# Kernel optimization log

Measured on AMD Instinct MI355X. Metric: run time of the kernel, lower is better.

## Reference

```python
import jax, jax.numpy as jnp
import numpy as np

POSE_IDS = np.array([0, 4, 8, 12, 16])
BN_EPS = 1e-5


def setup_inputs() -> dict:
    key = jax.random.key(0)
    ks = jax.random.split(key, 8)
    N, C, H, W = 64, 2048, 24, 12
    P, Cl = 5, 256
    Cm = C + P * Cl  # 3328
    return {
        "x": jax.random.normal(ks[0], (N, C, H, W), jnp.float32),
        "poses": jax.random.uniform(ks[1], (N, 17, 4), jnp.float32),
        "local_w": jax.random.normal(ks[2], (P, Cl, C), jnp.float32) * 0.02,
        "local_b": jnp.zeros((P, Cl), jnp.float32),
        "local_gamma": jnp.ones((P, Cl), jnp.float32),
        "local_beta": jnp.zeros((P, Cl), jnp.float32),
        "local_mean": jax.random.normal(ks[3], (P, Cl), jnp.float32) * 0.1,
        "local_var": jax.random.uniform(ks[4], (P, Cl), jnp.float32, 0.5, 1.5),
        "merge_w": jax.random.normal(ks[5], (C, Cm), jnp.float32) * 0.02,
        "merge_b": jnp.zeros((C,), jnp.float32),
        "merge_gamma": jnp.ones((C,), jnp.float32),
        "merge_beta": jnp.zeros((C,), jnp.float32),
        "merge_mean": jax.random.normal(ks[6], (C,), jnp.float32) * 0.1,
        "merge_var": jax.random.uniform(ks[7], (C,), jnp.float32, 0.5, 1.5),
    }


def reference(x, poses, local_w, local_b, local_gamma, local_beta, local_mean,
              local_var, merge_w, merge_b, merge_gamma, merge_beta, merge_mean,
              merge_var):
    N, C, H, W = x.shape
    kp = poses[:, jnp.asarray(POSE_IDS), :]  # [N,P,4]
    # box = [left, top, w, h]; clamp to [0, 0.75]; scale whole box by confidence
    half = jnp.full_like(kp[..., 0], 0.5)
    box = jnp.stack([kp[..., 0] - 0.25, kp[..., 1] - 0.25, half, half], axis=-1)
    box = jnp.clip(box, 0.0, 0.75) * kp[..., 2:3]
    # integer ROI bounds on the feature grid (round-half-to-even like torch)
    xs = jnp.maximum(0, jnp.round(W * box[..., 0])).astype(jnp.int32)          # [N,P]
    xe = jnp.minimum(W - 1, jnp.round(W * (box[..., 0] + box[..., 2]))).astype(jnp.int32)
    ys = jnp.maximum(0, jnp.round(H * box[..., 1])).astype(jnp.int32)
    ye = jnp.minimum(H - 1, jnp.round(H * (box[..., 1] + box[..., 3]))).astype(jnp.int32)
    rows = jnp.arange(H)
    cols = jnp.arange(W)
    mh = (rows[None, None, :] >= ys[..., None]) & (rows[None, None, :] < ye[..., None])  # [N,P,H]
    mw = (cols[None, None, :] >= xs[..., None]) & (cols[None, None, :] < xe[..., None])  # [N,P,W]
    mask = (mh[..., :, None] & mw[..., None, :]).astype(x.dtype)  # [N,P,H,W]
    # masked average pool over the ROI (single pass over x)
    sums = jnp.einsum('nchw,nphw->npc', x, mask)
    area = ((ye - ys) * (xe - xs)).astype(x.dtype)
    avg = sums / jnp.where(area > 0, area, 1.0)[..., None]  # [N,P,C], 0 for empty ROIs
    # per-part 1x1 conv + BN(eval) + ReLU -> [N,P,Cl]
    loc = jnp.einsum('npc,pkc->npk', avg, local_w) + local_b[None]
    loc = (loc - local_mean[None]) * (local_gamma[None] / jnp.sqrt(local_var[None] + BN_EPS)) + local_beta[None]
    loc = jax.nn.relu(loc)
    # global max pool -> [N,C]
    gfeat = x.max(axis=(2, 3))
    cat = jnp.concatenate([loc.reshape(N, -1), gfeat], axis=1)  # [N, P*Cl + C]
    # merge 1x1 conv + BN(eval) + ReLU
    y = cat @ merge_w.T + merge_b
    y = (y - merge_mean) * (merge_gamma / jnp.sqrt(merge_var + BN_EPS)) + merge_beta
    y = jax.nn.relu(y)
    # F.normalize(p=2, dim=1)
    norm = jnp.linalg.norm(y, axis=1, keepdims=True)
    return y / jnp.maximum(norm, 1e-12)
```

## Files before the change

kernel.cpp:

```cpp
#include <hip/hip_runtime.h>

#define N_   64
#define C_   2048
#define HW_  288
#define P_   5
#define CM_  3328
#define LOC_ 1280
#define SEGC 8
#define SEGM 13

#define PITCH  28
#define WPITCH 72

typedef __attribute__((ext_vector_type(8))) short bf16x8;
typedef __attribute__((ext_vector_type(4))) float f32x4;

__device__ __forceinline__ unsigned short f2bf(float f) {
  unsigned u = __float_as_uint(f);
  u = (u + 0x7FFFu + ((u >> 16) & 1u)) >> 16;
  return (unsigned short)u;
}
__device__ __forceinline__ unsigned pack2(float lo, float hi) {
  return (unsigned)f2bf(lo) | ((unsigned)f2bf(hi) << 16);
}

__global__ __launch_bounds__(256) void kB(const float* __restrict__ x,
    const float* __restrict__ poses,
    unsigned short* __restrict__ avgB, unsigned short* __restrict__ catB) {
  __shared__ float lds[2][256 * PITCH];
  const int t  = threadIdx.x;
  const int n  = blockIdx.x >> 3;
  const int cb = (blockIdx.x & 7) << 8;
  const int chbase = n * C_ + cb;

  unsigned MH[P_], MW[P_];
  float INV[P_];
  const float* kpn = poses + (size_t)n * 68;
#pragma unroll
  for (int p = 0; p < P_; ++p) {
    const float* kp = kpn + 16 * p;
    float px = kp[0], py = kp[1], z = kp[2];
    float bx = fminf(fmaxf(px - 0.25f, 0.f), 0.75f) * z;
    float by = fminf(fmaxf(py - 0.25f, 0.f), 0.75f) * z;
    float bw = 0.5f * z;
    float bh = 0.5f * z;
    int xs = (int)fmaxf(0.f,  rintf(12.f * bx));
    int xe = (int)fminf(11.f, rintf(12.f * (bx + bw)));
    int ys = (int)fmaxf(0.f,  rintf(24.f * by));
    int ye = (int)fminf(23.f, rintf(24.f * (by + bh)));
    MH[p] = ((1u << ye) - 1u) & ~((1u << ys) - 1u);
    MW[p] = ((1u << xe) - 1u) & ~((1u << xs) - 1u);
    int area = (ye - ys) * (xe - xs);
    INV[p] = area > 0 ? 1.f / (float)area : 1.f;
  }

  const float4* x4 = (const float4*)x;
  size_t gbase[6];
  int    loff[6];
#pragma unroll
  for (int k = 0; k < 6; ++k) {
    unsigned flat = k * 256 + t;
    unsigned cl = flat / 6u;
    unsigned j  = flat - 6u * cl;
    gbase[k] = (size_t)(chbase + cl) * 72 + j;
    loff[k]  = cl * PITCH + 4 * j;
  }

  float4 rg[6];
  auto loadRegs = [&](int ci) {
#pragma unroll
    for (int k = 0; k < 6; ++k) rg[k] = x4[gbase[k] + ci * 6];
  };
  auto writeRegs = [&](int db) {
#pragma unroll
    for (int k = 0; k < 6; ++k) *(float4*)&lds[db][loff[k]] = rg[k];
  };

  float s[P_] = {0.f, 0.f, 0.f, 0.f, 0.f};
  float mx = -3.402823466e+38f;

  loadRegs(0);
  writeRegs(0);
  __syncthreads();
  for (int ci = 0; ci < 12; ++ci) {
    if (ci + 1 < 12) loadRegs(ci + 1);
    const float* row = &lds[ci & 1][t * PITCH];
#pragma unroll
    for (int r = 0; r < 2; ++r) {
      int h = 2 * ci + r;
      float4 a = *(const float4*)(row + r * 12 + 0);
      float4 b = *(const float4*)(row + r * 12 + 4);
      float4 c = *(const float4*)(row + r * 12 + 8);
      float m1 = fmaxf(fmaxf(a.x, a.y), fmaxf(a.z, a.w));
      float m2 = fmaxf(fmaxf(b.x, b.y), fmaxf(b.z, b.w));
      float m3 = fmaxf(fmaxf(c.x, c.y), fmaxf(c.z, c.w));
      mx = fmaxf(mx, fmaxf(m1, fmaxf(m2, m3)));
#pragma unroll
      for (int p = 0; p < P_; ++p) {
        unsigned cm = ((MH[p] >> h) & 1u) ? MW[p] : 0u;
        if (cm) {
          float t0 = ((cm & 0x001u) ? a.x : 0.f) + ((cm & 0x002u) ? a.y : 0.f);
          float t1 = ((cm & 0x004u) ? a.z : 0.f) + ((cm & 0x008u) ? a.w : 0.f);
          float t2 = ((cm & 0x010u) ? b.x : 0.f) + ((cm & 0x020u) ? b.y : 0.f);
          float t3 = ((cm & 0x040u) ? b.z : 0.f) + ((cm & 0x080u) ? b.w : 0.f);
          float t4 = ((cm & 0x100u) ? c.x : 0.f) + ((cm & 0x200u) ? c.y : 0.f);
          float t5 = ((cm & 0x400u) ? c.z : 0.f) + ((cm & 0x800u) ? c.w : 0.f);
          s[p] += ((t0 + t1) + (t2 + t3)) + (t4 + t5);
        }
      }
    }
    if (ci + 1 < 12) {
      writeRegs((ci + 1) & 1);
      __syncthreads();
    }
  }

  int c = cb + t;
  catB[(size_t)n * CM_ + LOC_ + c] = f2bf(mx);
#pragma unroll
  for (int p = 0; p < P_; ++p)
    avgB[((size_t)n * 5 + p) * C_ + c] = f2bf(s[p] * INV[p]);
}

__device__ __forceinline__ void mfma_seg(const uint4* __restrict__ aRow,
                                         const float4* __restrict__ wRow,
                                         unsigned short* As, unsigned short* Ws,
                                         f32x4 acc[4]) {
  const int t  = threadIdx.x;
  const int kq = t & 3;
  const int row = t >> 2;
  const int w  = t >> 6;
  const int l  = t & 63;
  unsigned short* aw = &As[row * WPITCH + kq * 16];
  unsigned short* ww = &Ws[row * WPITCH + kq * 16];
  const int arow16 = (16 * w + (l & 15)) * WPITCH + (l >> 4) * 8;
  const int brow16 = (l & 15) * WPITCH + (l >> 4) * 8;
  for (int g = 0; g < 4; ++g) {
    uint4 a0 = aRow[g * 8 + 0], a1 = aRow[g * 8 + 1];
    float4 w0 = wRow[g * 16 + 0], w1 = wRow[g * 16 + 1],
           w2 = wRow[g * 16 + 2], w3 = wRow[g * 16 + 3];
    uint4 pw0, pw1;
    pw0.x = pack2(w0.x, w0.y); pw0.y = pack2(w0.z, w0.w);
    pw0.z = pack2(w1.x, w1.y); pw0.w = pack2(w1.z, w1.w);
    pw1.x = pack2(w2.x, w2.y); pw1.y = pack2(w2.z, w2.w);
    pw1.z = pack2(w3.x, w3.y); pw1.w = pack2(w3.z, w3.w);
    if (g) __syncthreads();
    *(uint4*)aw = a0; *(uint4*)(aw + 8) = a1;
    *(uint4*)ww = pw0; *(uint4*)(ww + 8) = pw1;
    __syncthreads();
#pragma unroll
    for (int s = 0; s < 2; ++s) {
      bf16x8 af = *(const bf16x8*)&As[arow16 + s * 32];
#pragma unroll
      for (int jm = 0; jm < 4; ++jm) {
        bf16x8 bf = *(const bf16x8*)&Ws[jm * 16 * WPITCH + brow16 + s * 32];
        acc[jm] = __builtin_amdgcn_mfma_f32_16x16x32_bf16(af, bf, acc[jm], 0, 0, 0);
      }
    }
  }
}

__global__ __launch_bounds__(256) void kC(const unsigned short* __restrict__ avgB,
                                          const float* __restrict__ local_w,
                                          float* __restrict__ locP) {
  __shared__ unsigned short As[64 * WPITCH];
  __shared__ unsigned short Ws[64 * WPITCH];
  int b  = blockIdx.x;
  int p  = b >> 5;
  int kt = (b >> 3) & 3;
  int sg = b & 7;
  const int t = threadIdx.x, row = t >> 2, kq = t & 3, w = t >> 6, l = t & 63;
  const uint4*  aRow = (const uint4*)avgB + ((size_t)row * 5 + p) * 256 + sg * 32 + kq * 2;
  const float4* wRow = (const float4*)(local_w + ((size_t)p * 256 + kt * 64 + row) * C_
                                       + sg * 256 + kq * 16);
  f32x4 acc[4] = {{0,0,0,0},{0,0,0,0},{0,0,0,0},{0,0,0,0}};
  mfma_seg(aRow, wRow, As, Ws, acc);
  float* outp = locP + (size_t)sg * (N_ * LOC_);
#pragma unroll
  for (int jm = 0; jm < 4; ++jm)
#pragma unroll
    for (int r = 0; r < 4; ++r)
      outp[(size_t)(16 * w + (l >> 4) * 4 + r) * LOC_ + p * 256 + kt * 64 + jm * 16 + (l & 15)]
        = acc[jm][r];
}

__global__ __launch_bounds__(256) void kC2(const float* __restrict__ locP,
    const float* __restrict__ lb, const float* __restrict__ lg, const float* __restrict__ lbe,
    const float* __restrict__ lm, const float* __restrict__ lv,
    unsigned short* __restrict__ catB) {
  int i = blockIdx.x * 256 + threadIdx.x;
  int n = i / LOC_;
  int q = i - n * LOC_;
  float s = 0.f;
#pragma unroll
  for (int sg = 0; sg < SEGC; ++sg) s += locP[(size_t)sg * (N_ * LOC_) + i];
  float sc = lg[q] / sqrtf(lv[q] + 1e-5f);
  float v = (s + lb[q] - lm[q]) * sc + lbe[q];
  catB[(size_t)n * CM_ + q] = f2bf(fmaxf(v, 0.f));
}

__global__ __launch_bounds__(256) void kD(const unsigned short* __restrict__ catB,
                                          const float* __restrict__ merge_w,
                                          float* __restrict__ mrgP) {
  __shared__ unsigned short As[64 * WPITCH];
  __shared__ unsigned short Ws[64 * WPITCH];
  int b  = blockIdx.x;
  int jt = b / SEGM;
  int sg = b - jt * SEGM;
  const int t = threadIdx.x, row = t >> 2, kq = t & 3, w = t >> 6, l = t & 63;
  const uint4*  aRow = (const uint4*)catB + (size_t)row * 416 + sg * 32 + kq * 2;
  const float4* wRow = (const float4*)(merge_w + (size_t)(jt * 64 + row) * CM_
                                       + sg * 256 + kq * 16);
  f32x4 acc[4] = {{0,0,0,0},{0,0,0,0},{0,0,0,0},{0,0,0,0}};
  mfma_seg(aRow, wRow, As, Ws, acc);
  float* outp = mrgP + (size_t)sg * (N_ * C_);
#pragma unroll
  for (int jm = 0; jm < 4; ++jm)
#pragma unroll
    for (int r = 0; r < 4; ++r)
      outp[(size_t)(16 * w + (l >> 4) * 4 + r) * C_ + jt * 64 + jm * 16 + (l & 15)]
        = acc[jm][r];
}

__global__ __launch_bounds__(256) void kE(const float* __restrict__ mrgP,
    const float* __restrict__ mb, const float* __restrict__ mg, const float* __restrict__ mbe,
    const float* __restrict__ mm, const float* __restrict__ mv,
    float* __restrict__ out) {
  int n = blockIdx.x, t = threadIdx.x;
  float z[8]; float ss = 0.f;
#pragma unroll
  for (int r = 0; r < 8; ++r) {
    int j = t + (r << 8);
    float y = 0.f;
#pragma unroll
    for (int sg = 0; sg < SEGM; ++sg) y += mrgP[(size_t)sg * (N_ * C_) + (size_t)n * C_ + j];
    float sc = mg[j] / sqrtf(mv[j] + 1e-5f);
    float v = (y + mb[j] - mm[j]) * sc + mbe[j];
    v = fmaxf(v, 0.f);
    z[r] = v; ss += v * v;
  }
#pragma unroll
  for (int off = 32; off; off >>= 1) ss += __shfl_xor(ss, off, 64);
  __shared__ float red[4];
  if ((t & 63) == 0) red[t >> 6] = ss;
  __syncthreads();
  float tot = red[0] + red[1] + red[2] + red[3];
  float inv = 1.f / fmaxf(sqrtf(tot), 1e-12f);
#pragma unroll
  for (int r = 0; r < 8; ++r) out[(size_t)n * C_ + t + (r << 8)] = z[r] * inv;
}

extern "C" void kernel_launch(void* const* d_in, const int* in_sizes, int n_in,
                              void* d_out, int out_size, void* d_ws, size_t ws_size,
                              hipStream_t stream) {
  const float* x          = (const float*)d_in[0];
  const float* poses      = (const float*)d_in[1];
  const float* local_w    = (const float*)d_in[2];
  const float* local_b    = (const float*)d_in[3];
  const float* local_g    = (const float*)d_in[4];
  const float* local_be   = (const float*)d_in[5];
  const float* local_m    = (const float*)d_in[6];
  const float* local_v    = (const float*)d_in[7];
  const float* merge_w    = (const float*)d_in[8];
  const float* merge_b    = (const float*)d_in[9];
  const float* merge_g    = (const float*)d_in[10];
  const float* merge_be   = (const float*)d_in[11];
  const float* merge_m    = (const float*)d_in[12];
  const float* merge_v    = (const float*)d_in[13];

  char* ws = (char*)d_ws;
  unsigned short* catB = (unsigned short*)ws;
  unsigned short* avgB = (unsigned short*)(ws + 425984);
  float* locP = (float*)(ws + 1736704);
  float* mrgP = (float*)(ws + 4358144);

  kB<<<512, 256, 0, stream>>>(x, poses, avgB, catB);
  kC<<<20 * SEGC, 256, 0, stream>>>(avgB, local_w, locP);
  kC2<<<(N_ * LOC_) / 256, 256, 0, stream>>>(locP, local_b, local_g, local_be,
                                             local_m, local_v, catB);
  kD<<<32 * SEGM, 256, 0, stream>>>(catB, merge_w, mrgP);
  kE<<<N_, 256, 0, stream>>>(mrgP, merge_b, merge_g, merge_be, merge_m, merge_v,
                             (float*)d_out);
}
```

Measured before the change: 294.7 us.

## Fuse all five stages into one cooperative persistent kernel with grid syncs

Replaces the five separate kernel launches with a single cooperative kernel of 256 blocks that runs each stage in turn, separated by grid-wide barriers. The aim is to remove launch overhead and the gaps between kernels. In exchange, the pooling and merge-GEMM stages now loop over work units with only 256 blocks instead of 512/416. That can lower parallelism and latency hiding, and the grid syncs add their own cost.

```diff
diff --git a/kernel.cpp b/kernel.cpp
--- a/kernel.cpp
+++ b/kernel.cpp
@@ -1,8 +1,10 @@
 #include <hip/hip_runtime.h>
+#include <hip/hip_cooperative_groups.h>
+
+namespace cg = cooperative_groups;
 
 #define N_   64
 #define C_   2048
-#define HW_  288
 #define P_   5
 #define CM_  3328
 #define LOC_ 1280
@@ -22,104 +24,6 @@
 }
 __device__ __forceinline__ unsigned pack2(float lo, float hi) {
   return (unsigned)f2bf(lo) | ((unsigned)f2bf(hi) << 16);
-}
-
-__global__ __launch_bounds__(256) void kB(const float* __restrict__ x,
-    const float* __restrict__ poses,
-    unsigned short* __restrict__ avgB, unsigned short* __restrict__ catB) {
-  __shared__ float lds[2][256 * PITCH];
-  const int t  = threadIdx.x;
-  const int n  = blockIdx.x >> 3;
-  const int cb = (blockIdx.x & 7) << 8;
-  const int chbase = n * C_ + cb;
-
-  unsigned MH[P_], MW[P_];
-  float INV[P_];
-  const float* kpn = poses + (size_t)n * 68;
-#pragma unroll
-  for (int p = 0; p < P_; ++p) {
-    const float* kp = kpn + 16 * p;
-    float px = kp[0], py = kp[1], z = kp[2];
-    float bx = fminf(fmaxf(px - 0.25f, 0.f), 0.75f) * z;
-    float by = fminf(fmaxf(py - 0.25f, 0.f), 0.75f) * z;
-    float bw = 0.5f * z;
-    float bh = 0.5f * z;
-    int xs = (int)fmaxf(0.f,  rintf(12.f * bx));
-    int xe = (int)fminf(11.f, rintf(12.f * (bx + bw)));
-    int ys = (int)fmaxf(0.f,  rintf(24.f * by));
-    int ye = (int)fminf(23.f, rintf(24.f * (by + bh)));
-    MH[p] = ((1u << ye) - 1u) & ~((1u << ys) - 1u);
-    MW[p] = ((1u << xe) - 1u) & ~((1u << xs) - 1u);
-    int area = (ye - ys) * (xe - xs);
-    INV[p] = area > 0 ? 1.f / (float)area : 1.f;
-  }
-
-  const float4* x4 = (const float4*)x;
-  size_t gbase[6];
-  int    loff[6];
-#pragma unroll
-  for (int k = 0; k < 6; ++k) {
-    unsigned flat = k * 256 + t;
-    unsigned cl = flat / 6u;
-    unsigned j  = flat - 6u * cl;
-    gbase[k] = (size_t)(chbase + cl) * 72 + j;
-    loff[k]  = cl * PITCH + 4 * j;
-  }
-
-  float4 rg[6];
-  auto loadRegs = [&](int ci) {
-#pragma unroll
-    for (int k = 0; k < 6; ++k) rg[k] = x4[gbase[k] + ci * 6];
-  };
-  auto writeRegs = [&](int db) {
-#pragma unroll
-    for (int k = 0; k < 6; ++k) *(float4*)&lds[db][loff[k]] = rg[k];
-  };
-
-  float s[P_] = {0.f, 0.f, 0.f, 0.f, 0.f};
-  float mx = -3.402823466e+38f;
-
-  loadRegs(0);
-  writeRegs(0);
-  __syncthreads();
-  for (int ci = 0; ci < 12; ++ci) {
-    if (ci + 1 < 12) loadRegs(ci + 1);
-    const float* row = &lds[ci & 1][t * PITCH];
-#pragma unroll
-    for (int r = 0; r < 2; ++r) {
-      int h = 2 * ci + r;
-      float4 a = *(const float4*)(row + r * 12 + 0);
-      float4 b = *(const float4*)(row + r * 12 + 4);
-      float4 c = *(const float4*)(row + r * 12 + 8);
-      float m1 = fmaxf(fmaxf(a.x, a.y), fmaxf(a.z, a.w));
-      float m2 = fmaxf(fmaxf(b.x, b.y), fmaxf(b.z, b.w));
-      float m3 = fmaxf(fmaxf(c.x, c.y), fmaxf(c.z, c.w));
-      mx = fmaxf(mx, fmaxf(m1, fmaxf(m2, m3)));
-#pragma unroll
-      for (int p = 0; p < P_; ++p) {
-        unsigned cm = ((MH[p] >> h) & 1u) ? MW[p] : 0u;
-        if (cm) {
-          float t0 = ((cm & 0x001u) ? a.x : 0.f) + ((cm & 0x002u) ? a.y : 0.f);
-          float t1 = ((cm & 0x004u) ? a.z : 0.f) + ((cm & 0x008u) ? a.w : 0.f);
-          float t2 = ((cm & 0x010u) ? b.x : 0.f) + ((cm & 0x020u) ? b.y : 0.f);
-          float t3 = ((cm & 0x040u) ? b.z : 0.f) + ((cm & 0x080u) ? b.w : 0.f);
-          float t4 = ((cm & 0x100u) ? c.x : 0.f) + ((cm & 0x200u) ? c.y : 0.f);
-          float t5 = ((cm & 0x400u) ? c.z : 0.f) + ((cm & 0x800u) ? c.w : 0.f);
-          s[p] += ((t0 + t1) + (t2 + t3)) + (t4 + t5);
-        }
-      }
-    }
-    if (ci + 1 < 12) {
-      writeRegs((ci + 1) & 1);
-      __syncthreads();
-    }
-  }
-
-  int c = cb + t;
-  catB[(size_t)n * CM_ + LOC_ + c] = f2bf(mx);
-#pragma unroll
-  for (int p = 0; p < P_; ++p)
-    avgB[((size_t)n * 5 + p) * C_ + c] = f2bf(s[p] * INV[p]);
 }
 
 __device__ __forceinline__ void mfma_seg(const uint4* __restrict__ aRow,
@@ -144,7 +48,7 @@
     pw0.z = pack2(w1.x, w1.y); pw0.w = pack2(w1.z, w1.w);
     pw1.x = pack2(w2.x, w2.y); pw1.y = pack2(w2.z, w2.w);
     pw1.z = pack2(w3.x, w3.y); pw1.w = pack2(w3.z, w3.w);
-    if (g) __syncthreads();
+    __syncthreads();
     *(uint4*)aw = a0; *(uint4*)(aw + 8) = a1;
     *(uint4*)ww = pw0; *(uint4*)(ww + 8) = pw1;
     __syncthreads();
@@ -160,94 +64,205 @@
   }
 }
 
-__global__ __launch_bounds__(256) void kC(const unsigned short* __restrict__ avgB,
-                                          const float* __restrict__ local_w,
-                                          float* __restrict__ locP) {
-  __shared__ unsigned short As[64 * WPITCH];
-  __shared__ unsigned short Ws[64 * WPITCH];
-  int b  = blockIdx.x;
-  int p  = b >> 5;
-  int kt = (b >> 3) & 3;
-  int sg = b & 7;
-  const int t = threadIdx.x, row = t >> 2, kq = t & 3, w = t >> 6, l = t & 63;
-  const uint4*  aRow = (const uint4*)avgB + ((size_t)row * 5 + p) * 256 + sg * 32 + kq * 2;
-  const float4* wRow = (const float4*)(local_w + ((size_t)p * 256 + kt * 64 + row) * C_
-                                       + sg * 256 + kq * 16);
-  f32x4 acc[4] = {{0,0,0,0},{0,0,0,0},{0,0,0,0},{0,0,0,0}};
-  mfma_seg(aRow, wRow, As, Ws, acc);
-  float* outp = locP + (size_t)sg * (N_ * LOC_);
-#pragma unroll
-  for (int jm = 0; jm < 4; ++jm)
-#pragma unroll
-    for (int r = 0; r < 4; ++r)
-      outp[(size_t)(16 * w + (l >> 4) * 4 + r) * LOC_ + p * 256 + kt * 64 + jm * 16 + (l & 15)]
-        = acc[jm][r];
-}
-
-__global__ __launch_bounds__(256) void kC2(const float* __restrict__ locP,
-    const float* __restrict__ lb, const float* __restrict__ lg, const float* __restrict__ lbe,
-    const float* __restrict__ lm, const float* __restrict__ lv,
-    unsigned short* __restrict__ catB) {
-  int i = blockIdx.x * 256 + threadIdx.x;
-  int n = i / LOC_;
-  int q = i - n * LOC_;
-  float s = 0.f;
-#pragma unroll
-  for (int sg = 0; sg < SEGC; ++sg) s += locP[(size_t)sg * (N_ * LOC_) + i];
-  float sc = lg[q] / sqrtf(lv[q] + 1e-5f);
-  float v = (s + lb[q] - lm[q]) * sc + lbe[q];
-  catB[(size_t)n * CM_ + q] = f2bf(fmaxf(v, 0.f));
-}
-
-__global__ __launch_bounds__(256) void kD(const unsigned short* __restrict__ catB,
-                                          const float* __restrict__ merge_w,
-                                          float* __restrict__ mrgP) {
-  __shared__ unsigned short As[64 * WPITCH];
-  __shared__ unsigned short Ws[64 * WPITCH];
-  int b  = blockIdx.x;
-  int jt = b / SEGM;
-  int sg = b - jt * SEGM;
-  const int t = threadIdx.x, row = t >> 2, kq = t & 3, w = t >> 6, l = t & 63;
-  const uint4*  aRow = (const uint4*)catB + (size_t)row * 416 + sg * 32 + kq * 2;
-  const float4* wRow = (const float4*)(merge_w + (size_t)(jt * 64 + row) * CM_
-                                       + sg * 256 + kq * 16);
-  f32x4 acc[4] = {{0,0,0,0},{0,0,0,0},{0,0,0,0},{0,0,0,0}};
-  mfma_seg(aRow, wRow, As, Ws, acc);
-  float* outp = mrgP + (size_t)sg * (N_ * C_);
-#pragma unroll
-  for (int jm = 0; jm < 4; ++jm)
-#pragma unroll
-    for (int r = 0; r < 4; ++r)
-      outp[(size_t)(16 * w + (l >> 4) * 4 + r) * C_ + jt * 64 + jm * 16 + (l & 15)]
-        = acc[jm][r];
-}
-
-__global__ __launch_bounds__(256) void kE(const float* __restrict__ mrgP,
-    const float* __restrict__ mb, const float* __restrict__ mg, const float* __restrict__ mbe,
-    const float* __restrict__ mm, const float* __restrict__ mv,
+__global__ __launch_bounds__(256) void mega(
+    const float* __restrict__ x, const float* __restrict__ poses,
+    const float* __restrict__ local_w,
+    const float* __restrict__ lb, const float* __restrict__ lg,
+    const float* __restrict__ lbe, const float* __restrict__ lm,
+    const float* __restrict__ lv,
+    const float* __restrict__ merge_w,
+    const float* __restrict__ mb, const float* __restrict__ mg,
+    const float* __restrict__ mbe, const float* __restrict__ mm,
+    const float* __restrict__ mv,
+    unsigned short* __restrict__ avgB, unsigned short* __restrict__ catB,
+    float* __restrict__ locP, float* __restrict__ mrgP,
     float* __restrict__ out) {
-  int n = blockIdx.x, t = threadIdx.x;
-  float z[8]; float ss = 0.f;
-#pragma unroll
-  for (int r = 0; r < 8; ++r) {
-    int j = t + (r << 8);
-    float y = 0.f;
-#pragma unroll
-    for (int sg = 0; sg < SEGM; ++sg) y += mrgP[(size_t)sg * (N_ * C_) + (size_t)n * C_ + j];
-    float sc = mg[j] / sqrtf(mv[j] + 1e-5f);
-    float v = (y + mb[j] - mm[j]) * sc + mbe[j];
-    v = fmaxf(v, 0.f);
-    z[r] = v; ss += v * v;
-  }
-#pragma unroll
-  for (int off = 32; off; off >>= 1) ss += __shfl_xor(ss, off, 64);
-  __shared__ float red[4];
-  if ((t & 63) == 0) red[t >> 6] = ss;
-  __syncthreads();
-  float tot = red[0] + red[1] + red[2] + red[3];
-  float inv = 1.f / fmaxf(sqrtf(tot), 1e-12f);
-#pragma unroll
-  for (int r = 0; r < 8; ++r) out[(size_t)n * C_ + t + (r << 8)] = z[r] * inv;
+  __shared__ __align__(16) char smem[2 * 256 * PITCH * 4];
+  cg::grid_group grid = cg::this_grid();
+  const int b = blockIdx.x;
+  const int t = threadIdx.x;
+
+  {
+    float* ldsB = (float*)smem;
+    const float4* x4 = (const float4*)x;
+    for (int unit = b; unit < 512; unit += 256) {
+      const int n  = unit >> 3;
+      const int cb = (unit & 7) << 8;
+      const int chbase = n * C_ + cb;
+
+      unsigned MH[P_], MW[P_];
+      float INV[P_];
+      const float* kpn = poses + (size_t)n * 68;
+#pragma unroll
+      for (int p = 0; p < P_; ++p) {
+        const float* kp = kpn + 16 * p;
+        float px = kp[0], py = kp[1], z = kp[2];
+        float bx = fminf(fmaxf(px - 0.25f, 0.f), 0.75f) * z;
+        float by = fminf(fmaxf(py - 0.25f, 0.f), 0.75f) * z;
+        float bw = 0.5f * z;
+        float bh = 0.5f * z;
+        int xs = (int)fmaxf(0.f,  rintf(12.f * bx));
+        int xe = (int)fminf(11.f, rintf(12.f * (bx + bw)));
+        int ys = (int)fmaxf(0.f,  rintf(24.f * by));
+        int ye = (int)fminf(23.f, rintf(24.f * (by + bh)));
+        MH[p] = ((1u << ye) - 1u) & ~((1u << ys) - 1u);
+        MW[p] = ((1u << xe) - 1u) & ~((1u << xs) - 1u);
+        int area = (ye - ys) * (xe - xs);
+        INV[p] = area > 0 ? 1.f / (float)area : 1.f;
+      }
+
+      size_t gbase[6];
+      int    loff[6];
+#pragma unroll
+      for (int k = 0; k < 6; ++k) {
+        unsigned flat = k * 256 + t;
+        unsigned cl = flat / 6u;
+        unsigned j  = flat - 6u * cl;
+        gbase[k] = (size_t)(chbase + cl) * 72 + j;
+        loff[k]  = cl * PITCH + 4 * j;
+      }
+
+      float4 rg[6];
+      auto loadRegs = [&](int ci) {
+#pragma unroll
+        for (int k = 0; k < 6; ++k) rg[k] = x4[gbase[k] + ci * 6];
+      };
+      auto writeRegs = [&](int db) {
+#pragma unroll
+        for (int k = 0; k < 6; ++k) *(float4*)&ldsB[db * 256 * PITCH + loff[k]] = rg[k];
+      };
+
+      float s[P_] = {0.f, 0.f, 0.f, 0.f, 0.f};
+      float mx = -3.402823466e+38f;
+
+      __syncthreads();
+      loadRegs(0);
+      writeRegs(0);
+      __syncthreads();
+      for (int ci = 0; ci < 12; ++ci) {
+        if (ci + 1 < 12) loadRegs(ci + 1);
+        const float* row = &ldsB[(ci & 1) * 256 * PITCH + t * PITCH];
+#pragma unroll
+        for (int r = 0; r < 2; ++r) {
+          int h = 2 * ci + r;
+          float4 a = *(const float4*)(row + r * 12 + 0);
+          float4 bq = *(const float4*)(row + r * 12 + 4);
+          float4 c = *(const float4*)(row + r * 12 + 8);
+          float m1 = fmaxf(fmaxf(a.x, a.y), fmaxf(a.z, a.w));
+          float m2 = fmaxf(fmaxf(bq.x, bq.y), fmaxf(bq.z, bq.w));
+          float m3 = fmaxf(fmaxf(c.x, c.y), fmaxf(c.z, c.w));
+          mx = fmaxf(mx, fmaxf(m1, fmaxf(m2, m3)));
+#pragma unroll
+          for (int p = 0; p < P_; ++p) {
+            unsigned cm = ((MH[p] >> h) & 1u) ? MW[p] : 0u;
+            if (cm) {
+              float t0 = ((cm & 0x001u) ? a.x : 0.f) + ((cm & 0x002u) ? a.y : 0.f);
+              float t1 = ((cm & 0x004u) ? a.z : 0.f) + ((cm & 0x008u) ? a.w : 0.f);
+              float t2 = ((cm & 0x010u) ? bq.x : 0.f) + ((cm & 0x020u) ? bq.y : 0.f);
+              float t3 = ((cm & 0x040u) ? bq.z : 0.f) + ((cm & 0x080u) ? bq.w : 0.f);
+              float t4 = ((cm & 0x100u) ? c.x : 0.f) + ((cm & 0x200u) ? c.y : 0.f);
+              float t5 = ((cm & 0x400u) ? c.z : 0.f) + ((cm & 0x800u) ? c.w : 0.f);
+              s[p] += ((t0 + t1) + (t2 + t3)) + (t4 + t5);
+            }
+          }
+        }
+        if (ci + 1 < 12) {
+          writeRegs((ci + 1) & 1);
+          __syncthreads();
+        }
+      }
+
+      int c = cb + t;
+      catB[(size_t)n * CM_ + LOC_ + c] = f2bf(mx);
+#pragma unroll
+      for (int p = 0; p < P_; ++p)
+        avgB[((size_t)n * 5 + p) * C_ + c] = f2bf(s[p] * INV[p]);
+    }
+  }
+  grid.sync();
+
+  if (b < 160) {
+    unsigned short* As = (unsigned short*)smem;
+    unsigned short* Ws = As + 64 * WPITCH;
+    int p  = b >> 5;
+    int kt = (b >> 3) & 3;
+    int sg = b & 7;
+    const int row = t >> 2, kq = t & 3, w = t >> 6, l = t & 63;
+    const uint4*  aRow = (const uint4*)avgB + ((size_t)row * 5 + p) * 256 + sg * 32 + kq * 2;
+    const float4* wRow = (const float4*)(local_w + ((size_t)p * 256 + kt * 64 + row) * C_
+                                         + sg * 256 + kq * 16);
+    f32x4 acc[4] = {{0,0,0,0},{0,0,0,0},{0,0,0,0},{0,0,0,0}};
+    mfma_seg(aRow, wRow, As, Ws, acc);
+    float* outp = locP + (size_t)sg * (N_ * LOC_);
+#pragma unroll
+    for (int jm = 0; jm < 4; ++jm)
+#pragma unroll
+      for (int r = 0; r < 4; ++r)
+        outp[(size_t)(16 * w + (l >> 4) * 4 + r) * LOC_ + p * 256 + kt * 64 + jm * 16 + (l & 15)]
+          = acc[jm][r];
+  }
+  grid.sync();
+
+  for (int i = b * 256 + t; i < N_ * LOC_; i += 256 * 256) {
+    int n = i / LOC_;
+    int q = i - n * LOC_;
+    float s = 0.f;
+#pragma unroll
+    for (int sg = 0; sg < SEGC; ++sg) s += locP[(size_t)sg * (N_ * LOC_) + i];
+    float sc = lg[q] / sqrtf(lv[q] + 1e-5f);
+    float v = (s + lb[q] - lm[q]) * sc + lbe[q];
+    catB[(size_t)n * CM_ + q] = f2bf(fmaxf(v, 0.f));
+  }
+  grid.sync();
+
+  {
+    unsigned short* As = (unsigned short*)smem;
+    unsigned short* Ws = As + 64 * WPITCH;
+    for (int u = b; u < 32 * SEGM; u += 256) {
+      int jt = u / SEGM;
+      int sg = u - jt * SEGM;
+      const int row = t >> 2, kq = t & 3, w = t >> 6, l = t & 63;
+      const uint4*  aRow = (const uint4*)catB + (size_t)row * 416 + sg * 32 + kq * 2;
+      const float4* wRow = (const float4*)(merge_w + (size_t)(jt * 64 + row) * CM_
+                                           + sg * 256 + kq * 16);
+      f32x4 acc[4] = {{0,0,0,0},{0,0,0,0},{0,0,0,0},{0,0,0,0}};
+      mfma_seg(aRow, wRow, As, Ws, acc);
+      float* outp = mrgP + (size_t)sg * (N_ * C_);
+#pragma unroll
+      for (int jm = 0; jm < 4; ++jm)
+#pragma unroll
+        for (int r = 0; r < 4; ++r)
+          outp[(size_t)(16 * w + (l >> 4) * 4 + r) * C_ + jt * 64 + jm * 16 + (l & 15)]
+            = acc[jm][r];
+    }
+  }
+  grid.sync();
+
+  if (b < N_) {
+    int n = b;
+    float* red = (float*)smem;
+    float z[8]; float ss = 0.f;
+#pragma unroll
+    for (int r = 0; r < 8; ++r) {
+      int j = t + (r << 8);
+      float y = 0.f;
+#pragma unroll
+      for (int sg = 0; sg < SEGM; ++sg) y += mrgP[(size_t)sg * (N_ * C_) + (size_t)n * C_ + j];
+      float sc = mg[j] / sqrtf(mv[j] + 1e-5f);
+      float v = (y + mb[j] - mm[j]) * sc + mbe[j];
+      v = fmaxf(v, 0.f);
+      z[r] = v; ss += v * v;
+    }
+#pragma unroll
+    for (int off = 32; off; off >>= 1) ss += __shfl_xor(ss, off, 64);
+    __syncthreads();
+    if ((t & 63) == 0) red[t >> 6] = ss;
+    __syncthreads();
+    float tot = red[0] + red[1] + red[2] + red[3];
+    float inv = 1.f / fmaxf(sqrtf(tot), 1e-12f);
+#pragma unroll
+    for (int r = 0; r < 8; ++r) out[(size_t)n * C_ + t + (r << 8)] = z[r] * inv;
+  }
 }
 
 extern "C" void kernel_launch(void* const* d_in, const int* in_sizes, int n_in,
@@ -273,12 +288,14 @@
   unsigned short* avgB = (unsigned short*)(ws + 425984);
   float* locP = (float*)(ws + 1736704);
   float* mrgP = (float*)(ws + 4358144);
-
-  kB<<<512, 256, 0, stream>>>(x, poses, avgB, catB);
-  kC<<<20 * SEGC, 256, 0, stream>>>(avgB, local_w, locP);
-  kC2<<<(N_ * LOC_) / 256, 256, 0, stream>>>(locP, local_b, local_g, local_be,
-                                             local_m, local_v, catB);
-  kD<<<32 * SEGM, 256, 0, stream>>>(catB, merge_w, mrgP);
-  kE<<<N_, 256, 0, stream>>>(mrgP, merge_b, merge_g, merge_be, merge_m, merge_v,
-                             (float*)d_out);
-}
+  float* out  = (float*)d_out;
+
+  void* args[] = {
+    (void*)&x, (void*)&poses, (void*)&local_w,
+    (void*)&local_b, (void*)&local_g, (void*)&local_be, (void*)&local_m, (void*)&local_v,
+    (void*)&merge_w, (void*)&merge_b, (void*)&merge_g, (void*)&merge_be,
+    (void*)&merge_m, (void*)&merge_v,
+    (void*)&avgB, (void*)&catB, (void*)&locP, (void*)&mrgP, (void*)&out,
+  };
+  hipLaunchCooperativeKernel((const void*)mega, dim3(256), dim3(256), args, 0, stream);
+}
```

New measurement: 440.4 us. 49.4% more time.
